# Kernel tuning notes

Hardware: AMD Instinct MI355X
Metric: run time of the kernel (lower is better)

The kernel has to match this reference:

```python
import jax, jax.numpy as jnp
import numpy as np

B, T, C, H, N = 4, 4096, 1024, 16, 64
D_DECAY, D_AAA, D_MV, D_GATE = 64, 64, 32, 160
EPS_GN = 1e-5 * 8 ** 2  # GroupNorm eps = 1e-5 * head_size_divisor**2


def _k(i):
    return jax.random.fold_in(jax.random.key(0), i)


def setup_inputs():
    p = {}
    p["x"] = jax.random.normal(_k(1), (B, T, C), jnp.float32)
    p["v_first"] = jax.random.normal(_k(2), (B, T, C), jnp.float32)
    for i, name in enumerate(["x_r", "x_w", "x_k", "x_v", "x_a", "x_g"]):
        p[name] = jax.random.uniform(_k(10 + i), (1, 1, C), jnp.float32)
    p["w0"] = jnp.linspace(-7.0, -2.0, C, dtype=jnp.float32).reshape(1, 1, C) + 0.5
    p["w1"] = jax.random.normal(_k(20), (C, D_DECAY), jnp.float32) * 0.02
    p["w2"] = jax.random.normal(_k(21), (D_DECAY, C), jnp.float32) * 0.02
    p["a0"] = jax.random.normal(_k(22), (1, 1, C), jnp.float32) * 0.02
    p["a1"] = jax.random.normal(_k(23), (C, D_AAA), jnp.float32) * 0.02
    p["a2"] = jax.random.normal(_k(24), (D_AAA, C), jnp.float32) * 0.02
    p["v0"] = jnp.ones((1, 1, C), jnp.float32)
    p["v1"] = jax.random.normal(_k(25), (C, D_MV), jnp.float32) * 0.02
    p["v2"] = jax.random.normal(_k(26), (D_MV, C), jnp.float32) * 0.02
    p["g1"] = jax.random.normal(_k(27), (C, D_GATE), jnp.float32) * 0.02
    p["g2"] = jax.random.normal(_k(28), (D_GATE, C), jnp.float32) * 0.02
    p["k_k"] = jnp.full((1, 1, C), 0.85, jnp.float32)
    p["k_a"] = jnp.ones((1, 1, C), jnp.float32)
    p["r_k"] = jax.random.normal(_k(29), (H, N), jnp.float32) * 0.02
    s = 0.5 / C ** 0.5
    p["Wr"] = jax.random.uniform(_k(30), (C, C), jnp.float32, -s, s)
    p["Wk"] = jax.random.uniform(_k(31), (C, C), jnp.float32, -0.1 * s, 0.1 * s)
    p["Wv"] = jax.random.uniform(_k(32), (C, C), jnp.float32, -s, s)
    p["Wo"] = jax.random.uniform(_k(33), (C, C), jnp.float32, -s, s)
    p["ln_w"] = jnp.ones((C,), jnp.float32)
    p["ln_b"] = jnp.zeros((C,), jnp.float32)
    p["alpha"] = jnp.array(0.5, jnp.float32)
    return p


def _wkv_scan(ins, reverse):
    # ins: tuple of time-major (T,B,H,N) arrays: r, decay, k, v, a, b
    def step(S, inp):
        r_t, d_t, k_t, v_t, a_t, b_t = inp
        sa = jnp.einsum('bhij,bhj->bhi', S, a_t)  # in-context removal term
        S = (S * d_t[:, :, None, :]
             + sa[..., None] * b_t[:, :, None, :]
             + v_t[..., None] * k_t[:, :, None, :])
        return S, jnp.einsum('bhij,bhj->bhi', S, r_t)
    S0 = jnp.zeros((B, H, N, N), jnp.float32)
    return jax.lax.scan(step, S0, ins, reverse=reverse)[1]


def reference(x, v_first, x_r, x_w, x_k, x_v, x_a, x_g, w0, w1, w2, a0, a1, a2,
              v0, v1, v2, g1, g2, k_k, k_a, r_k, Wr, Wk, Wv, Wo, ln_w, ln_b, alpha):
    xx = jnp.pad(x, ((0, 0), (1, 0), (0, 0)))[:, :T, :] - x  # token shift
    xr = x + xx * x_r
    xw = x + xx * x_w
    xk = x + xx * x_k
    xv = x + xx * x_v
    xa = x + xx * x_a
    xg = x + xx * x_g
    r = xr @ Wr.T
    w = -jax.nn.softplus(-(w0 + jnp.tanh(xw @ w1) @ w2)) - 0.5
    k = xk @ Wk.T
    v = xv @ Wv.T
    v = v + (v_first - v) * jax.nn.sigmoid(v0 + (xv @ v1) @ v2)  # layer_id != 0
    a = jax.nn.sigmoid(a0 + (xa @ a1) @ a2)
    g = jax.nn.sigmoid(xg @ g1) @ g2
    kk = (k * k_k).reshape(B, T, H, N)
    kk = kk / jnp.maximum(jnp.linalg.norm(kk, axis=-1, keepdims=True), 1e-12)
    k = k * (1.0 + (a - 1.0) * k_a)
    rh = r.reshape(B, T, H, N)
    kh = k.reshape(B, T, H, N)
    vh = v.reshape(B, T, H, N)
    dec = jnp.exp(-jnp.exp(w.reshape(B, T, H, N)))  # per-channel decay
    ah = -kk
    bh = kk * a.reshape(B, T, H, N)
    tm = lambda z: jnp.transpose(z, (1, 0, 2, 3))  # -> (T,B,H,N)
    ins = (tm(rh), tm(dec), tm(kh), tm(vh), tm(ah), tm(bh))
    y_f = _wkv_scan(ins, reverse=False)
    y_b = _wkv_scan(ins, reverse=True)
    y = alpha * y_f + (1.0 - alpha) * y_b  # bidirectional blend (alpha)
    y = jnp.transpose(y, (1, 0, 2, 3))  # (B,T,H,N)
    mu = y.mean(-1, keepdims=True)
    var = y.var(-1, keepdims=True)
    y = (y - mu) / jnp.sqrt(var + EPS_GN)  # GroupNorm(H groups)
    y = y * ln_w.reshape(1, 1, H, N) + ln_b.reshape(1, 1, H, N)
    y = y + (rh * kh * r_k).sum(-1, keepdims=True) * vh
    out = (y.reshape(B, T, C) * g) @ Wo.T
    return (out, v_first)
```

## Files before the change

### kernel.cpp

```cpp
#include <hip/hip_runtime.h>
#include <hip/hip_bf16.h>
#include <math.h>

#define BB 4
#define TT 4096
#define CC 1024
#define HH 16
#define NN 64
#define BT (BB*TT)
#define EPS_GN 6.4e-4f
#define TMAX (TT-1)
#define LCH 64
#define CB 8
#define NB 8
#define STR 68

typedef __attribute__((ext_vector_type(8))) short bf16x8;
typedef __attribute__((ext_vector_type(4))) float f32x4;

__device__ __forceinline__ float sigmoidf_(float x) {
    return 1.0f / (1.0f + expf(-x));
}

__device__ __forceinline__ float waveReduceSum(float v) {
    #pragma unroll
    for (int off = 32; off > 0; off >>= 1)
        v += __shfl_xor(v, off, 64);
    return v;
}

__device__ __forceinline__ unsigned short f2bf(float f) {
    unsigned u = __float_as_uint(f);
    u += 0x7FFFu + ((u >> 16) & 1u);
    return (unsigned short)(u >> 16);
}
__device__ __forceinline__ float bf2f(unsigned short h) {
    return __uint_as_float(((unsigned)h) << 16);
}

__device__ __forceinline__ void gll16(const unsigned short* g, unsigned short* l) {
    __builtin_amdgcn_global_load_lds(
        (__attribute__((address_space(1))) void*)(g),
        (__attribute__((address_space(3))) void*)(l), 16, 0, 0);
}

template<int SA0,int SA1,int SB0,int SB1>
__device__ __forceinline__ void gemm64(const float* __restrict__ A,
                                       const float* __restrict__ B,
                                       float acc[4][4], int tr, int tc) {
    #pragma unroll 2
    for (int kx = 0; kx < 64; kx += 4) {
        float a_[4][4];
        if (SA0 == 1) {
            #pragma unroll
            for (int kk = 0; kk < 4; kk++) {
                float4 t = *(const float4*)&A[tr + (kx + kk) * SA1];
                a_[0][kk] = t.x; a_[1][kk] = t.y; a_[2][kk] = t.z; a_[3][kk] = t.w;
            }
        } else {
            #pragma unroll
            for (int r = 0; r < 4; r++) {
                float4 t = *(const float4*)&A[(tr + r) * SA0 + kx];
                a_[r][0] = t.x; a_[r][1] = t.y; a_[r][2] = t.z; a_[r][3] = t.w;
            }
        }
        float b_[4][4];
        if (SB0 == 1) {
            #pragma unroll
            for (int kk = 0; kk < 4; kk++) {
                float4 t = *(const float4*)&B[tc + (kx + kk) * SB1];
                b_[0][kk] = t.x; b_[1][kk] = t.y; b_[2][kk] = t.z; b_[3][kk] = t.w;
            }
        } else {
            #pragma unroll
            for (int cq = 0; cq < 4; cq++) {
                float4 t = *(const float4*)&B[(tc + cq) * SB0 + kx];
                b_[cq][0] = t.x; b_[cq][1] = t.y; b_[cq][2] = t.z; b_[cq][3] = t.w;
            }
        }
        #pragma unroll
        for (int r = 0; r < 4; r++)
            #pragma unroll
            for (int cq = 0; cq < 4; cq++)
                #pragma unroll
                for (int kk = 0; kk < 4; kk++)
                    acc[r][cq] = fmaf(a_[r][kk], b_[cq][kk], acc[r][cq]);
    }
}

__global__ __launch_bounds__(256) void conv_split_x3(
    const float* __restrict__ X,
    const float* __restrict__ mr, const float* __restrict__ mk,
    const float* __restrict__ mv,
    unsigned short* __restrict__ rH, unsigned short* __restrict__ rL,
    unsigned short* __restrict__ kH, unsigned short* __restrict__ kL,
    unsigned short* __restrict__ vH, unsigned short* __restrict__ vL)
{
    int g = blockIdx.x * 256 + threadIdx.x;
    int m = g >> 7;
    int k = (g & 127) * 8;
    const float* px = X + (size_t)m * CC + k;
    float xv8[8], pv[8];
    {
        float4 x0 = *(const float4*)px;
        float4 x1 = *(const float4*)(px + 4);
        xv8[0]=x0.x; xv8[1]=x0.y; xv8[2]=x0.z; xv8[3]=x0.w;
        xv8[4]=x1.x; xv8[5]=x1.y; xv8[6]=x1.z; xv8[7]=x1.w;
    }
    if ((m & (TT - 1)) == 0) {
        #pragma unroll
        for (int j = 0; j < 8; j++) pv[j] = 0.f;
    } else {
        float4 p0 = *(const float4*)(px - CC);
        float4 p1 = *(const float4*)(px - CC + 4);
        pv[0]=p0.x; pv[1]=p0.y; pv[2]=p0.z; pv[3]=p0.w;
        pv[4]=p1.x; pv[5]=p1.y; pv[6]=p1.z; pv[7]=p1.w;
    }
    const float* mixes[3] = {mr, mk, mv};
    unsigned short* His[3] = {rH, kH, vH};
    unsigned short* Los[3] = {rL, kL, vL};
    #pragma unroll
    for (int s = 0; s < 3; s++) {
        float4 m0 = *(const float4*)(mixes[s] + k);
        float4 m1 = *(const float4*)(mixes[s] + k + 4);
        float mv8[8] = {m0.x,m0.y,m0.z,m0.w,m1.x,m1.y,m1.z,m1.w};
        unsigned short hi[8], lo[8];
        #pragma unroll
        for (int j = 0; j < 8; j++) {
            float a = xv8[j] + (pv[j] - xv8[j]) * mv8[j];
            hi[j] = f2bf(a);
            lo[j] = f2bf(a - bf2f(hi[j]));
        }
        uint4 H, L;
        H.x = (unsigned)hi[0] | ((unsigned)hi[1] << 16);
        H.y = (unsigned)hi[2] | ((unsigned)hi[3] << 16);
        H.z = (unsigned)hi[4] | ((unsigned)hi[5] << 16);
        H.w = (unsigned)hi[6] | ((unsigned)hi[7] << 16);
        L.x = (unsigned)lo[0] | ((unsigned)lo[1] << 16);
        L.y = (unsigned)lo[2] | ((unsigned)lo[3] << 16);
        L.z = (unsigned)lo[4] | ((unsigned)lo[5] << 16);
        L.w = (unsigned)lo[6] | ((unsigned)lo[7] << 16);
        *(uint4*)(His[s] + (size_t)g * 8) = H;
        *(uint4*)(Los[s] + (size_t)g * 8) = L;
    }
}


__global__ __launch_bounds__(256) void conv_w4(
    const float* __restrict__ Wr, const float* __restrict__ Wk,
    const float* __restrict__ Wv, const float* __restrict__ Wo,
    unsigned short* __restrict__ Hi, unsigned short* __restrict__ Lo)
{
    int g = blockIdx.x * 256 + threadIdx.x;
    int y = blockIdx.y;
    const float* W = (y == 0) ? Wr : (y == 1) ? Wk : (y == 2) ? Wv : Wo;
    size_t doff = (size_t)y * CC * CC;
    int m = g >> 7;
    int k = (g & 127) * 8;
    const float* px = W + (size_t)m * CC + k;
    float a[8];
    {
        float4 x0 = *(const float4*)px;
        float4 x1 = *(const float4*)(px + 4);
        a[0]=x0.x; a[1]=x0.y; a[2]=x0.z; a[3]=x0.w;
        a[4]=x1.x; a[5]=x1.y; a[6]=x1.z; a[7]=x1.w;
    }
    unsigned short hi[8], lo[8];
    #pragma unroll
    for (int j = 0; j < 8; j++) {
        hi[j] = f2bf(a[j]);
        lo[j] = f2bf(a[j] - bf2f(hi[j]));
    }
    uint4 H, L;
    H.x = (unsigned)hi[0] | ((unsigned)hi[1] << 16);
    H.y = (unsigned)hi[2] | ((unsigned)hi[3] << 16);
    H.z = (unsigned)hi[4] | ((unsigned)hi[5] << 16);
    H.w = (unsigned)hi[6] | ((unsigned)hi[7] << 16);
    L.x = (unsigned)lo[0] | ((unsigned)lo[1] << 16);
    L.y = (unsigned)lo[2] | ((unsigned)lo[3] << 16);
    L.z = (unsigned)lo[4] | ((unsigned)lo[5] << 16);
    L.w = (unsigned)lo[6] | ((unsigned)lo[7] << 16);
    *(uint4*)(Hi + doff + (size_t)g * 8) = H;
    *(uint4*)(Lo + doff + (size_t)g * 8) = L;
}

__global__ __launch_bounds__(256) void conv_w2(
    const float* __restrict__ W, int K, int Kp,
    unsigned short* __restrict__ Hi, unsigned short* __restrict__ Lo)
{
    int idx = blockIdx.x * 256 + threadIdx.x;
    int nk8 = Kp >> 3;
    if (idx >= CC * nk8) return;
    int n = idx / nk8, k0 = (idx - n * nk8) * 8;
    unsigned short h8[8], l8[8];
    #pragma unroll
    for (int j = 0; j < 8; j++) {
        int k = k0 + j;
        float v = (k < K) ? W[(size_t)k * CC + n] : 0.f;
        h8[j] = f2bf(v);
        l8[j] = f2bf(v - bf2f(h8[j]));
    }
    uint4 H, L;
    H.x = (unsigned)h8[0] | ((unsigned)h8[1] << 16);
    H.y = (unsigned)h8[2] | ((unsigned)h8[3] << 16);
    H.z = (unsigned)h8[4] | ((unsigned)h8[5] << 16);
    H.w = (unsigned)h8[6] | ((unsigned)h8[7] << 16);
    L.x = (unsigned)l8[0] | ((unsigned)l8[1] << 16);
    L.y = (unsigned)l8[2] | ((unsigned)l8[3] << 16);
    L.z = (unsigned)l8[4] | ((unsigned)l8[5] << 16);
    L.w = (unsigned)l8[6] | ((unsigned)l8[7] << 16);
    *(uint4*)(Hi + (size_t)n * Kp + k0) = H;
    *(uint4*)(Lo + (size_t)n * Kp + k0) = L;
}

__global__ __launch_bounds__(256, 3) void gemm_split_bf16(
    const unsigned short* __restrict__ A0h, const unsigned short* __restrict__ A0l,
    const unsigned short* __restrict__ A1h, const unsigned short* __restrict__ A1l,
    const unsigned short* __restrict__ A2h, const unsigned short* __restrict__ A2l,
    const unsigned short* __restrict__ W4h, const unsigned short* __restrict__ W4l,
    float* __restrict__ O0, float* __restrict__ O1, float* __restrict__ O2,
    int wbase)
{
    __shared__ __align__(16) unsigned short lds[4][128 * 32];
    const int sel = blockIdx.y;
    const unsigned short* Ah = (sel == 0) ? A0h : (sel == 1) ? A1h : A2h;
    const unsigned short* Al = (sel == 0) ? A0l : (sel == 1) ? A1l : A2l;
    float* Out = (sel == 0) ? O0 : (sel == 1) ? O1 : O2;
    const unsigned short* Bh = W4h + (size_t)(wbase + sel) * CC * CC;
    const unsigned short* Bl = W4l + (size_t)(wbase + sel) * CC * CC;
    const int tid = threadIdx.x, lane = tid & 63, wave = tid >> 6;
    const int wm = (wave >> 1) * 64, wn = (wave & 1) * 64;
    const int wg = blockIdx.x;
    const int xcd = wg & 7;
    const int j = wg >> 3;
    const int m0 = ((j >> 3) * 8 + xcd) * 128;
    const int n0 = (j & 7) * 128;

    f32x4 acc[4][4];
    #pragma unroll
    for (int i = 0; i < 4; i++)
        #pragma unroll
        for (int jj = 0; jj < 4; jj++)
            acc[i][jj] = (f32x4){0.f, 0.f, 0.f, 0.f};

    for (int k0 = 0; k0 < CC; k0 += 32) {
        #pragma unroll
        for (int p = 0; p < 4; p++) {
            const unsigned short* sbase = (p == 0) ? Ah : (p == 1) ? Al
                                        : (p == 2) ? Bh : Bl;
            const int rbase = (p < 2) ? m0 : n0;
            #pragma unroll
            for (int i = 0; i < 2; i++) {
                int slot = i * 256 + wave * 64 + lane;
                int row = slot >> 2, gsl = slot & 3;
                const unsigned short* src = sbase
                    + (size_t)(rbase + row) * CC + k0 + ((gsl ^ (row & 3)) * 8);
                gll16(src, &lds[p][(size_t)(i * 256 + wave * 64) * 8]);
            }
        }
        __syncthreads();

        const int gk = lane >> 4;
        bf16x8 bhf[4], blf[4];
        #pragma unroll
        for (int nt = 0; nt < 4; nt++) {
            int col = wn + nt * 16 + (lane & 15);
            int el = col * 32 + ((gk ^ (col & 3)) * 8);
            bhf[nt] = *(const bf16x8*)&lds[2][el];
            blf[nt] = *(const bf16x8*)&lds[3][el];
        }
        #pragma unroll
        for (int mt = 0; mt < 4; mt++) {
            int row = wm + mt * 16 + (lane & 15);
            int el = row * 32 + ((gk ^ (row & 3)) * 8);
            bf16x8 ahf = *(const bf16x8*)&lds[0][el];
            bf16x8 alf = *(const bf16x8*)&lds[1][el];
            #pragma unroll
            for (int nt = 0; nt < 4; nt++) {
                acc[mt][nt] = __builtin_amdgcn_mfma_f32_16x16x32_bf16(
                    ahf, bhf[nt], acc[mt][nt], 0, 0, 0);
                acc[mt][nt] = __builtin_amdgcn_mfma_f32_16x16x32_bf16(
                    alf, bhf[nt], acc[mt][nt], 0, 0, 0);
                acc[mt][nt] = __builtin_amdgcn_mfma_f32_16x16x32_bf16(
                    ahf, blf[nt], acc[mt][nt], 0, 0, 0);
            }
        }
        __syncthreads();
    }
    #pragma unroll
    for (int mt = 0; mt < 4; mt++)
        #pragma unroll
        for (int nt = 0; nt < 4; nt++) {
            int col = n0 + wn + nt * 16 + (lane & 15);
            #pragma unroll
            for (int r = 0; r < 4; r++) {
                int row = m0 + wm + mt * 16 + (lane >> 4) * 4 + r;
                Out[(size_t)row * CC + col] = acc[mt][nt][r];
            }
        }
}

__global__ __launch_bounds__(256) void lora1_all(
    const float* __restrict__ X,
    const float* __restrict__ w1, const float* __restrict__ a1,
    const float* __restrict__ v1, const float* __restrict__ g1,
    const float* __restrict__ xw, const float* __restrict__ xa,
    const float* __restrict__ xv, const float* __restrict__ xg,
    unsigned short* __restrict__ awh, unsigned short* __restrict__ awl,
    unsigned short* __restrict__ aah, unsigned short* __restrict__ aal,
    unsigned short* __restrict__ avh, unsigned short* __restrict__ avl,
    unsigned short* __restrict__ agh, unsigned short* __restrict__ agl)
{
    const int y = blockIdx.y;
    const float* W; const float* mix; unsigned short *Hi, *Lo;
    int Ncols, n0, epi, Kp;
    if (y == 0)      { W=w1; mix=xw; Hi=awh; Lo=awl; Ncols=64;  n0=0;          epi=1; Kp=64;  }
    else if (y == 1) { W=a1; mix=xa; Hi=aah; Lo=aal; Ncols=64;  n0=0;          epi=0; Kp=64;  }
    else if (y == 2) { W=v1; mix=xv; Hi=avh; Lo=avl; Ncols=32;  n0=0;          epi=0; Kp=64;  }
    else             { W=g1; mix=xg; Hi=agh; Lo=agl; Ncols=160; n0=(y-3)*64;   epi=2; Kp=192; }

    __shared__ float As[8][64];
    __shared__ float Bs[8][64];
    const int tid = threadIdx.x;
    const int m0 = blockIdx.x * 64;
    const int sr  = tid >> 1;
    const int skq = (tid & 1) * 4;
    const int t2  = tid - 128;
    const int bkr = t2 >> 4;
    const int bnq = (t2 & 15) * 4;
    const int tm = (tid >> 3) * 2;
    const int tn = (tid & 7) * 8;

    float acc[2][8];
    #pragma unroll
    for (int i = 0; i < 2; i++)
        #pragma unroll
        for (int j = 0; j < 8; j++) acc[i][j] = 0.f;

    auto ldAm = [&](int gm, int gk) -> float4 {
        const float* px = X + (size_t)gm * CC + gk;
        float4 xvv = *(const float4*)px;
        float4 pv;
        if ((gm & (TT - 1)) == 0) pv = make_float4(0.f, 0.f, 0.f, 0.f);
        else pv = *(const float4*)(px - CC);
        float4 mv = *(const float4*)(mix + gk);
        xvv.x += (pv.x - xvv.x) * mv.x;
        xvv.y += (pv.y - xvv.y) * mv.y;
        xvv.z += (pv.z - xvv.z) * mv.z;
        xvv.w += (pv.w - xvv.w) * mv.w;
        return xvv;
    };

    float4 aR = make_float4(0.f, 0.f, 0.f, 0.f);
    float4 bR = make_float4(0.f, 0.f, 0.f, 0.f);
    if (tid < 128) {
        aR = ldAm(m0 + sr, skq);
    } else {
        int gn = n0 + bnq;
        bR = (gn < Ncols) ? *(const float4*)(W + (size_t)bkr * Ncols + gn)
                          : make_float4(0.f, 0.f, 0.f, 0.f);
    }

    for (int k0 = 0; k0 < CC; k0 += 8) {
        __syncthreads();
        if (tid < 128) {
            As[skq + 0][sr] = aR.x;
            As[skq + 1][sr] = aR.y;
            As[skq + 2][sr] = aR.z;
            As[skq + 3][sr] = aR.w;
        } else {
            *(float4*)&Bs[bkr][bnq] = bR;
        }
        __syncthreads();

        if (k0 + 8 < CC) {
            if (tid < 128) {
                aR = ldAm(m0 + sr, k0 + 8 + skq);
            } else {
                int gn = n0 + bnq;
                bR = (gn < Ncols) ? *(const float4*)(W + (size_t)(k0 + 8 + bkr) * Ncols + gn)
                                  : make_float4(0.f, 0.f, 0.f, 0.f);
            }
        }

        #pragma unroll
        for (int kk = 0; kk < 8; ++kk) {
            float av[2], bv[8];
            av[0] = As[kk][tm];
            av[1] = As[kk][tm + 1];
            *(float4*)&bv[0] = *(const float4*)&Bs[kk][tn];
            *(float4*)&bv[4] = *(const float4*)&Bs[kk][tn + 4];
            #pragma unroll
            for (int i = 0; i < 2; i++)
                #pragma unroll
                for (int j = 0; j < 8; j++)
                    acc[i][j] = fmaf(av[i], bv[j], acc[i][j]);
        }
    }

    #pragma unroll
    for (int i = 0; i < 2; i++) {
        int gm = m0 + tm + i;
        int gn = n0 + tn;
        if (gn < Kp) {
            unsigned short h8[8], l8[8];
            #pragma unroll
            for (int j = 0; j < 8; j++) {
                float v = 0.f;
                if (gn + j < Ncols) {
                    v = acc[i][j];
                    if (epi == 1) v = tanhf(v);
                    else if (epi == 2) v = sigmoidf_(v);
                }
                h8[j] = f2bf(v);
                l8[j] = f2bf(v - bf2f(h8[j]));
            }
            uint4 H, L;
            H.x = (unsigned)h8[0] | ((unsigned)h8[1] << 16);
            H.y = (unsigned)h8[2] | ((unsigned)h8[3] << 16);
            H.z = (unsigned)h8[4] | ((unsigned)h8[5] << 16);
            H.w = (unsigned)h8[6] | ((unsigned)h8[7] << 16);
            L.x = (unsigned)l8[0] | ((unsigned)l8[1] << 16);
            L.y = (unsigned)l8[2] | ((unsigned)l8[3] << 16);
            L.z = (unsigned)l8[4] | ((unsigned)l8[5] << 16);
            L.w = (unsigned)l8[6] | ((unsigned)l8[7] << 16);
            *(uint4*)(Hi + (size_t)gm * Kp + gn) = H;
            *(uint4*)(Lo + (size_t)gm * Kp + gn) = L;
        }
    }
}

__global__ __launch_bounds__(256, 3) void lora2_mfma(
    const unsigned short* __restrict__ awh, const unsigned short* __restrict__ awl,
    const unsigned short* __restrict__ aah, const unsigned short* __restrict__ aal,
    const unsigned short* __restrict__ avh, const unsigned short* __restrict__ avl,
    const unsigned short* __restrict__ agh, const unsigned short* __restrict__ agl,
    const unsigned short* __restrict__ w2h, const unsigned short* __restrict__ w2l,
    const unsigned short* __restrict__ a2h, const unsigned short* __restrict__ a2l,
    const unsigned short* __restrict__ v2h, const unsigned short* __restrict__ v2l,
    const unsigned short* __restrict__ g2h, const unsigned short* __restrict__ g2l,
    const float* __restrict__ w0, const float* __restrict__ a0v,
    const float* __restrict__ v0v, const float* __restrict__ v_first,
    float* __restrict__ decb, float* __restrict__ ab,
    float* __restrict__ vbuf, float* __restrict__ gb)
{
    __shared__ __align__(16) unsigned short lds[24576];
    const int z = blockIdx.z;
    const unsigned short *Ah, *Al, *Bh, *Bl; int Kp;
    if (z == 0)      { Ah = awh; Al = awl; Bh = w2h; Bl = w2l; Kp = 64;  }
    else if (z == 1) { Ah = aah; Al = aal; Bh = a2h; Bl = a2l; Kp = 64;  }
    else if (z == 2) { Ah = avh; Al = avl; Bh = v2h; Bl = v2l; Kp = 64;  }
    else             { Ah = agh; Al = agl; Bh = g2h; Bl = g2l; Kp = 192; }

    const int tid = threadIdx.x, lane = tid & 63, wave = tid >> 6;
    const int wm = (wave >> 1) * 64, wn = (wave & 1) * 32;
    const int m0 = blockIdx.x * 128, n0 = blockIdx.y * 64;

    f32x4 acc[4][2];
    #pragma unroll
    for (int i = 0; i < 4; i++)
        #pragma unroll
        for (int jj = 0; jj < 2; jj++)
            acc[i][jj] = (f32x4){0.f, 0.f, 0.f, 0.f};

    for (int k0 = 0; k0 < Kp; k0 += 64) {
        #pragma unroll
        for (int p = 0; p < 2; p++) {
            const unsigned short* sbase = (p == 0) ? Ah : Al;
            #pragma unroll
            for (int i = 0; i < 4; i++) {
                int slot = i * 256 + wave * 64 + lane;
                int row = slot >> 3, gsl = slot & 7;
                const unsigned short* src = sbase
                    + (size_t)(m0 + row) * Kp + k0 + ((gsl ^ (row & 7)) * 8);
                gll16(src, &lds[(size_t)(p * 8192) + (size_t)(i * 256 + wave * 64) * 8]);
            }
        }
        #pragma unroll
        for (int p = 0; p < 2; p++) {
            const unsigned short* sbase = (p == 0) ? Bh : Bl;
            #pragma unroll
            for (int i = 0; i < 2; i++) {
                int slot = i * 256 + wave * 64 + lane;
                int row = slot >> 3, gsl = slot & 7;
                const unsigned short* src = sbase
                    + (size_t)(n0 + row) * Kp + k0 + ((gsl ^ (row & 7)) * 8);
                gll16(src, &lds[(size_t)(16384 + p * 4096) + (size_t)(i * 256 + wave * 64) * 8]);
            }
        }
        __syncthreads();

        #pragma unroll
        for (int ks = 0; ks < 2; ks++) {
            bf16x8 bhf[2], blf[2];
            #pragma unroll
            for (int nt = 0; nt < 2; nt++) {
                int col = wn + nt * 16 + (lane & 15);
                int gk = ks * 4 + (lane >> 4);
                int el = col * 64 + ((gk ^ (col & 7)) * 8);
                bhf[nt] = *(const bf16x8*)&lds[16384 + el];
                blf[nt] = *(const bf16x8*)&lds[20480 + el];
            }
            #pragma unroll
            for (int mt = 0; mt < 4; mt++) {
                int row = wm + mt * 16 + (lane & 15);
                int gk = ks * 4 + (lane >> 4);
                int el = row * 64 + ((gk ^ (row & 7)) * 8);
                bf16x8 ahf = *(const bf16x8*)&lds[el];
                bf16x8 alf = *(const bf16x8*)&lds[8192 + el];
                #pragma unroll
                for (int nt = 0; nt < 2; nt++) {
                    acc[mt][nt] = __builtin_amdgcn_mfma_f32_16x16x32_bf16(
                        ahf, bhf[nt], acc[mt][nt], 0, 0, 0);
                    acc[mt][nt] = __builtin_amdgcn_mfma_f32_16x16x32_bf16(
                        alf, bhf[nt], acc[mt][nt], 0, 0, 0);
                    acc[mt][nt] = __builtin_amdgcn_mfma_f32_16x16x32_bf16(
                        ahf, blf[nt], acc[mt][nt], 0, 0, 0);
                }
            }
        }
        __syncthreads();
    }
    float* cf = (float*)&lds[0];
    #pragma unroll
    for (int mt = 0; mt < 4; mt++)
        #pragma unroll
        for (int nt = 0; nt < 2; nt++)
            #pragma unroll
            for (int r = 0; r < 4; r++) {
                int row = wm + mt * 16 + (lane >> 4) * 4 + r;
                int col = wn + nt * 16 + (lane & 15);
                cf[row * 68 + col] = acc[mt][nt][r];
            }
    __syncthreads();
    #pragma unroll
    for (int i = 0; i < 8; i++) {
        int idx = tid + 256 * i;
        int row = idx >> 4, c4 = (idx & 15) * 4;
        float4 v = *(float4*)&cf[row * 68 + c4];
        int gm = m0 + row;
        int c = n0 + c4;
        size_t off = (size_t)gm * CC + c;
        if (z == 0) {
            float4 w0q = *(const float4*)(w0 + c);
            float4 o;
            o.x = expf(-expf(-log1pf(expf(-(w0q.x + v.x))) - 0.5f));
            o.y = expf(-expf(-log1pf(expf(-(w0q.y + v.y))) - 0.5f));
            o.z = expf(-expf(-log1pf(expf(-(w0q.z + v.z))) - 0.5f));
            o.w = expf(-expf(-log1pf(expf(-(w0q.w + v.w))) - 0.5f));
            *(float4*)&decb[off] = o;
        } else if (z == 1) {
            float4 a0q = *(const float4*)(a0v + c);
            float4 o;
            o.x = sigmoidf_(a0q.x + v.x);
            o.y = sigmoidf_(a0q.y + v.y);
            o.z = sigmoidf_(a0q.z + v.z);
            o.w = sigmoidf_(a0q.w + v.w);
            *(float4*)&ab[off] = o;
        } else if (z == 2) {
            float4 v0q = *(const float4*)(v0v + c);
            float4 vr = *(const float4*)&vbuf[off];
            float4 vf = *(const float4*)&v_first[off];
            float4 o;
            o.x = vr.x + (vf.x - vr.x) * sigmoidf_(v0q.x + v.x);
            o.y = vr.y + (vf.y - vr.y) * sigmoidf_(v0q.y + v.y);
            o.z = vr.z + (vf.z - vr.z) * sigmoidf_(v0q.z + v.z);
            o.w = vr.w + (vf.w - vr.w) * sigmoidf_(v0q.w + v.w);
            *(float4*)&vbuf[off] = o;
        } else {
            *(float4*)&gb[off] = v;
        }
    }
}

__global__ __launch_bounds__(256) void wkvA(
    const float* __restrict__ kb, const float* __restrict__ ab,
    const float* __restrict__ vb, const float* __restrict__ decb,
    const float* __restrict__ k_k, const float* __restrict__ k_a,
    float* __restrict__ Gb, float* __restrict__ Ub,
    float* __restrict__ Bpb, float* __restrict__ Kpb,
    float* __restrict__ wcb, int cb)
{
    __shared__ __align__(16) float sAp[64 * STR];
    __shared__ __align__(16) float sBp[64 * STR];
    __shared__ __align__(16) float sKp[64 * STR];
    __shared__ __align__(16) float sT [64 * STR];
    __shared__ float sSeg[4][64];
    const int inst = blockIdx.x;
    const int bhd = inst >> 3, lc = inst & 7;
    const int dir = bhd & 1, bh = bhd >> 1, b = bh >> 4, h = bh & 15;
    const int c64 = (cb * CB + lc) * LCH;
    const int tid = threadIdx.x;
    const int lane = tid & 63, seg = tid >> 6;
    const int ch = h * 64 + lane;
    const size_t gbase = (size_t)inst * 4096;

    float loc[16];
    {
        float run = 1.f;
        #pragma unroll
        for (int i = 0; i < 16; i++) {
            int p = seg * 16 + i;
            int t = dir ? (TMAX - (c64 + p)) : (c64 + p);
            float d = decb[((size_t)(b * TT + t)) * CC + ch];
            run *= d; loc[i] = run;
        }
        sSeg[seg][lane] = run;
    }
    __syncthreads();
    float pre = 1.f;
    for (int s2 = 0; s2 < seg; ++s2) pre *= sSeg[s2][lane];
    {
        const float kkl = k_k[ch], kal = k_a[ch];
        #pragma unroll
        for (int i = 0; i < 16; i++) {
            int p = seg * 16 + i;
            int t = dir ? (TMAX - (c64 + p)) : (c64 + p);
            size_t ra = ((size_t)(b * TT + t)) * CC + ch;
            float kraw = kb[ra], asig = ab[ra];
            float kkv = kraw * kkl;
            float s2 = waveReduceSum(kkv * kkv);
            float kkn = kkv / fmaxf(sqrtf(s2), 1e-12f);
            float wc = loc[i] * pre;
            float wx = (i == 0) ? pre : loc[i - 1] * pre;
            float apv = -kkn * wx;
            float bpv = kkn * asig / wc;
            float kpv = kraw * (1.f + (asig - 1.f) * kal) / wc;
            sAp[lane * STR + p] = apv;
            sBp[lane * STR + p] = bpv;
            sKp[lane * STR + p] = kpv;
            Bpb[gbase + p * 64 + lane] = bpv;
            Kpb[gbase + p * 64 + lane] = kpv;
            wcb[gbase + p * 64 + lane] = wc;
        }
    }
    __syncthreads();

    const int tr = (tid >> 4) * 4, tc = (tid & 15) * 4;
    {
        float acc[4][4] = {};
        gemm64<1, STR, 1, STR>(sAp, sKp, acc, tr, tc);
        #pragma unroll
        for (int r = 0; r < 4; r++)
            #pragma unroll
            for (int cq = 0; cq < 4; cq++)
                sT[(tr + r) * STR + tc + cq] = (tc + cq < tr + r) ? acc[r][cq] : 0.f;
    }
    __syncthreads();
    {
        float accY[4][4] = {};
        const float* vbase = vb + ((size_t)(b * TT + (dir ? (TMAX - c64) : c64))) * CC
                           + h * 64 + tc;
        const ptrdiff_t vstep = dir ? -(ptrdiff_t)CC : (ptrdiff_t)CC;
        #pragma unroll 2
        for (int j4 = 0; j4 < 64; j4 += 4) {
            float a_[4][4];
            #pragma unroll
            for (int r = 0; r < 4; r++) {
                float4 t4 = *(const float4*)&sT[(tr + r) * STR + j4];
                a_[r][0] = t4.x; a_[r][1] = t4.y; a_[r][2] = t4.z; a_[r][3] = t4.w;
            }
            float4 vq[4];
            #pragma unroll
            for (int kk = 0; kk < 4; kk++)
                vq[kk] = *(const float4*)(vbase + (ptrdiff_t)(j4 + kk) * vstep);
            #pragma unroll
            for (int r = 0; r < 4; r++) {
                accY[r][0] = fmaf(a_[r][0], vq[0].x, fmaf(a_[r][1], vq[1].x,
                             fmaf(a_[r][2], vq[2].x, fmaf(a_[r][3], vq[3].x, accY[r][0]))));
                accY[r][1] = fmaf(a_[r][0], vq[0].y, fmaf(a_[r][1], vq[1].y,
                             fmaf(a_[r][2], vq[2].y, fmaf(a_[r][3], vq[3].y, accY[r][1]))));
                accY[r][2] = fmaf(a_[r][0], vq[0].z, fmaf(a_[r][1], vq[1].z,
                             fmaf(a_[r][2], vq[2].z, fmaf(a_[r][3], vq[3].z, accY[r][2]))));
                accY[r][3] = fmaf(a_[r][0], vq[0].w, fmaf(a_[r][1], vq[1].w,
                             fmaf(a_[r][2], vq[2].w, fmaf(a_[r][3], vq[3].w, accY[r][3]))));
            }
        }
        #pragma unroll
        for (int r = 0; r < 4; r++)
            #pragma unroll
            for (int cq = 0; cq < 4; cq++)
                sKp[(tr + r) * STR + tc + cq] = accY[r][cq];
    }
    __syncthreads();
    {
        float acc[4][4] = {};
        gemm64<1, STR, 1, STR>(sAp, sBp, acc, tr, tc);
        #pragma unroll
        for (int r = 0; r < 4; r++)
            #pragma unroll
            for (int cq = 0; cq < 4; cq++)
                sT[(tr + r) * STR + tc + cq] = (tc + cq < tr + r) ? acc[r][cq] : 0.f;
    }
    __syncthreads();
    if (tid < 64) {
        for (int r = 0; r < 64; ++r) {
            float acc = 0.f;
            for (int s = 0; s < r; ++s)
                acc = fmaf(sT[r * STR + s], sBp[s * STR + tid], acc);
            sBp[r * STR + tid] = (r == tid) ? 1.f : acc;
        }
    }
    __syncthreads();
    {
        float accG[4][4] = {};
        gemm64<STR, 1, STR, 1>(sBp, sAp, accG, tr, tc);
        float accU[4][4] = {};
        gemm64<STR, 1, 1, STR>(sBp, sKp, accU, tr, tc);
        #pragma unroll
        for (int r = 0; r < 4; r++) {
            *(float4*)&Gb[gbase + (tr + r) * 64 + tc] =
                make_float4(accG[r][0], accG[r][1], accG[r][2], accG[r][3]);
            *(float4*)&Ub[gbase + (tr + r) * 64 + tc] =
                make_float4(accU[r][0], accU[r][1], accU[r][2], accU[r][3]);
        }
    }
}

__global__ __launch_bounds__(256) void wkvB(
    const float* __restrict__ vb,
    const float* __restrict__ Gb, float* __restrict__ Ub,
    const float* __restrict__ Bpb, const float* __restrict__ Kpb,
    const float* __restrict__ wcb, float* __restrict__ S0b,
    float* __restrict__ Scur, int cb)
{
    __shared__ __align__(16) float sS[64 * STR];
    __shared__ __align__(16) float sG[64 * STR];
    __shared__ __align__(16) float sU[64 * STR];
    __shared__ __align__(16) float sB[64 * STR];
    __shared__ __align__(16) float sK[64 * STR];
    __shared__ __align__(16) float sV[64 * STR];
    const int bhd = blockIdx.x;
    const int dir = bhd & 1, bh = bhd >> 1, b = bh >> 4, h = bh & 15;
    const int tid = threadIdx.x;
    const int tr = (tid >> 4) * 4, tc = (tid & 15) * 4;

    for (int i = tid; i < 4096; i += 256)
        sS[(i >> 6) * STR + (i & 63)] = Scur[(size_t)bhd * 4096 + i];
    __syncthreads();

    for (int lc = 0; lc < CB; ++lc) {
        const int inst = bhd * CB + lc;
        const size_t gbase = (size_t)inst * 4096;
        const int c64 = (cb * CB + lc) * LCH;
        for (int i = tid; i < 4096; i += 256) {
            int rr = i >> 6, jj = i & 63;
            sG[rr * STR + jj] = Gb[gbase + i];
            sB[rr * STR + jj] = Bpb[gbase + i];
            sK[rr * STR + jj] = Kpb[gbase + i];
            int t = dir ? (TMAX - (c64 + rr)) : (c64 + rr);
            sV[rr * STR + jj] = vb[((size_t)(b * TT + t)) * CC + h * 64 + jj];
            S0b[gbase + i] = sS[rr * STR + jj];
        }
        __syncthreads();
        {
            float acc[4][4];
            #pragma unroll
            for (int r = 0; r < 4; r++) {
                float4 u0 = *(const float4*)&Ub[gbase + (tr + r) * 64 + tc];
                acc[r][0] = u0.x; acc[r][1] = u0.y; acc[r][2] = u0.z; acc[r][3] = u0.w;
            }
            gemm64<STR, 1, STR, 1>(sG, sS, acc, tr, tc);
            #pragma unroll
            for (int r = 0; r < 4; r++) {
                #pragma unroll
                for (int cq = 0; cq < 4; cq++) sU[(tr + r) * STR + tc + cq] = acc[r][cq];
                *(float4*)&Ub[gbase + (tr + r) * 64 + tc] =
                    make_float4(acc[r][0], acc[r][1], acc[r][2], acc[r][3]);
            }
        }
        __syncthreads();
        {
            float acc[4][4] = {};
            gemm64<1, STR, 1, STR>(sU, sB, acc, tr, tc);
            gemm64<1, STR, 1, STR>(sV, sK, acc, tr, tc);
            float w63[4];
            #pragma unroll
            for (int cq = 0; cq < 4; cq++) w63[cq] = wcb[gbase + 63 * 64 + tc + cq];
            #pragma unroll
            for (int r = 0; r < 4; r++)
                #pragma unroll
                for (int cq = 0; cq < 4; cq++) {
                    float sv = sS[(tr + r) * STR + tc + cq];
                    acc[r][cq] = (sv + acc[r][cq]) * w63[cq];
                }
            #pragma unroll
            for (int r = 0; r < 4; r++)
                #pragma unroll
                for (int cq = 0; cq < 4; cq++)
                    sS[(tr + r) * STR + tc + cq] = acc[r][cq];
        }
        __syncthreads();
    }
    for (int i = tid; i < 4096; i += 256)
        Scur[(size_t)bhd * 4096 + i] = sS[(i >> 6) * STR + (i & 63)];
}

__global__ __launch_bounds__(256) void wkvC(
    const float* __restrict__ rb, const float* __restrict__ vb,
    const float* __restrict__ Bpb, const float* __restrict__ Kpb,
    const float* __restrict__ Ub, const float* __restrict__ S0b,
    const float* __restrict__ wcb, const float* __restrict__ alpha_p,
    float* __restrict__ yb, int cb)
{
    __shared__ __align__(16) float sR[64 * STR];
    __shared__ __align__(16) float sO[64 * STR];
    __shared__ __align__(16) float sT2[64 * STR];
    const int inst = blockIdx.x;
    const int bhd = inst >> 3, lc = inst & 7;
    const int dir = bhd & 1, bh = bhd >> 1, b = bh >> 4, h = bh & 15;
    const int c64 = (cb * CB + lc) * LCH;
    const int tid = threadIdx.x, lane = tid & 63, seg = tid >> 6;
    const size_t gbase = (size_t)inst * 4096;
    const float alpha = alpha_p[0];
    const float wscale = dir ? (1.f - alpha) : alpha;
    const bool first = (cb < NB / 2);

    #pragma unroll
    for (int i = 0; i < 16; i++) {
        int p = seg * 16 + i;
        int t = dir ? (TMAX - (c64 + p)) : (c64 + p);
        size_t ra = ((size_t)(b * TT + t)) * CC + h * 64 + lane;
        float wc = wcb[gbase + p * 64 + lane];
        sR[lane * STR + p] = rb[ra] * wc;
        sO[lane * STR + p] = Bpb[gbase + p * 64 + lane];
    }
    __syncthreads();
    const int tr = (tid >> 4) * 4, tc = (tid & 15) * 4;
    float accO[4][4] = {};
    {
        float acc[4][4] = {};
        gemm64<1, STR, 1, STR>(sR, sO, acc, tr, tc);
        #pragma unroll
        for (int r = 0; r < 4; r++)
            #pragma unroll
            for (int cq = 0; cq < 4; cq++)
                sT2[(tr + r) * STR + tc + cq] = (tc + cq <= tr + r) ? acc[r][cq] : 0.f;
    }
    __syncthreads();
    for (int i = tid; i < 4096; i += 256)
        sO[(i >> 6) * STR + (i & 63)] = Ub[gbase + i];
    __syncthreads();
    gemm64<STR, 1, 1, STR>(sT2, sO, accO, tr, tc);
    __syncthreads();
    #pragma unroll
    for (int i = 0; i < 16; i++) {
        int p = seg * 16 + i;
        sO[lane * STR + p] = Kpb[gbase + p * 64 + lane];
    }
    __syncthreads();
    {
        float acc[4][4] = {};
        gemm64<1, STR, 1, STR>(sR, sO, acc, tr, tc);
        #pragma unroll
        for (int r = 0; r < 4; r++)
            #pragma unroll
            for (int cq = 0; cq < 4; cq++)
                sT2[(tr + r) * STR + tc + cq] = (tc + cq <= tr + r) ? acc[r][cq] : 0.f;
    }
    __syncthreads();
    #pragma unroll
    for (int i = 0; i < 16; i++) {
        int p = seg * 16 + i;
        int t = dir ? (TMAX - (c64 + p)) : (c64 + p);
        sO[p * STR + lane] = vb[((size_t)(b * TT + t)) * CC + h * 64 + lane];
    }
    __syncthreads();
    gemm64<STR, 1, 1, STR>(sT2, sO, accO, tr, tc);
    __syncthreads();
    for (int i = tid; i < 4096; i += 256)
        sO[(i >> 6) * STR + (i & 63)] = S0b[gbase + i];
    __syncthreads();
    gemm64<1, STR, STR, 1>(sR, sO, accO, tr, tc);
    #pragma unroll
    for (int r = 0; r < 4; r++) {
        int p = tr + r;
        int t = dir ? (TMAX - (c64 + p)) : (c64 + p);
        float* yp = &yb[((size_t)(b * TT + t)) * CC + h * 64 + tc];
        float4 o;
        if (first) {
            o.x = wscale * accO[r][0];
            o.y = wscale * accO[r][1];
            o.z = wscale * accO[r][2];
            o.w = wscale * accO[r][3];
        } else {
            float4 old = *(float4*)yp;
            o.x = old.x + wscale * accO[r][0];
            o.y = old.y + wscale * accO[r][1];
            o.z = old.z + wscale * accO[r][2];
            o.w = old.w + wscale * accO[r][3];
        }
        *(float4*)yp = o;
    }
}

__global__ __launch_bounds__(256) void post_kernel(
    const float* __restrict__ yb, const float* __restrict__ rbv,
    const float* __restrict__ kbv, const float* __restrict__ abv,
    const float* __restrict__ vbv, const float* __restrict__ gbv,
    const float* __restrict__ kaw, const float* __restrict__ r_k,
    const float* __restrict__ ln_w, const float* __restrict__ ln_b,
    unsigned short* __restrict__ zh, unsigned short* __restrict__ zl)
{
    const int t = blockIdx.x;
    const int tid = threadIdx.x;
    const size_t base = (size_t)t * CC;
    #pragma unroll
    for (int j = 0; j < 4; j++) {
        int c = tid + 256 * j;
        float y = yb[base + c];
        float s1 = waveReduceSum(y);
        float s2 = waveReduceSum(y * y);
        float mu = s1 * (1.0f / 64.0f);
        float var = s2 * (1.0f / 64.0f) - mu * mu;
        float yn = (y - mu) * rsqrtf(var + EPS_GN);
        yn = yn * ln_w[c] + ln_b[c];
        float rv = rbv[base + c];
        float kf = kbv[base + c] * (1.0f + (abv[base + c] - 1.0f) * kaw[c]);
        float vv = vbv[base + c];
        float dot = waveReduceSum(rv * kf * r_k[c]);
        yn += dot * vv;
        float z = yn * gbv[base + c];
        unsigned short h = f2bf(z);
        zh[base + c] = h;
        zl[base + c] = f2bf(z - bf2f(h));
    }
}

extern "C" void kernel_launch(void* const* d_in, const int* in_sizes, int n_in,
                              void* d_out, int out_size, void* d_ws, size_t ws_size,
                              hipStream_t stream)
{
    (void)in_sizes; (void)n_in; (void)out_size; (void)ws_size;
    const float* x      = (const float*)d_in[0];
    const float* vfirst = (const float*)d_in[1];
    const float* x_r    = (const float*)d_in[2];
    const float* x_w    = (const float*)d_in[3];
    const float* x_k    = (const float*)d_in[4];
    const float* x_v    = (const float*)d_in[5];
    const float* x_a    = (const float*)d_in[6];
    const float* x_g    = (const float*)d_in[7];
    const float* w0     = (const float*)d_in[8];
    const float* w1     = (const float*)d_in[9];
    const float* w2     = (const float*)d_in[10];
    const float* a0     = (const float*)d_in[11];
    const float* a1     = (const float*)d_in[12];
    const float* a2     = (const float*)d_in[13];
    const float* v0     = (const float*)d_in[14];
    const float* v1     = (const float*)d_in[15];
    const float* v2     = (const float*)d_in[16];
    const float* g1     = (const float*)d_in[17];
    const float* g2     = (const float*)d_in[18];
    const float* k_k    = (const float*)d_in[19];
    const float* k_a    = (const float*)d_in[20];
    const float* r_k    = (const float*)d_in[21];
    const float* Wr     = (const float*)d_in[22];
    const float* Wk     = (const float*)d_in[23];
    const float* Wv     = (const float*)d_in[24];
    const float* Wo     = (const float*)d_in[25];
    const float* ln_w   = (const float*)d_in[26];
    const float* ln_b   = (const float*)d_in[27];
    const float* alpha  = (const float*)d_in[28];

    const size_t SZ = (size_t)BT * CC;
    const size_t CHB = (size_t)1024 * 4096;
    float* ws   = (float*)d_ws;
    float* rb   = ws + 0 * SZ;
    float* kb   = ws + 1 * SZ;
    float* vb   = ws + 2 * SZ;
    float* decb = ws + 3 * SZ;
    float* ab   = ws + 4 * SZ;
    float* actf = ws + 5 * SZ;
    unsigned short* awh = (unsigned short*)actf;
    unsigned short* awl = awh + (size_t)BT * 64;
    unsigned short* aah = awl + (size_t)BT * 64;
    unsigned short* aal = aah + (size_t)BT * 64;
    unsigned short* avh = aal + (size_t)BT * 64;
    unsigned short* avl = avh + (size_t)BT * 64;
    unsigned short* agh = avl + (size_t)BT * 64;
    unsigned short* agl = agh + (size_t)BT * 192;
    float* Gb   = actf + (size_t)BT * 384;
    float* Ub   = Gb + CHB;
    float* Bpb  = Ub + CHB;
    float* Kpb  = Bpb + CHB;
    float* S0b  = Kpb + CHB;
    float* wcb  = S0b + CHB;
    float* Scur = wcb + CHB;
    unsigned short* W4h = (unsigned short*)(Scur + (size_t)128 * 4096);
    unsigned short* W4l = W4h + (size_t)CC * CC * 4;
    unsigned short* w2th = W4l + (size_t)CC * CC * 4;
    unsigned short* w2tl = w2th + (size_t)CC * 64;
    unsigned short* a2th = w2tl + (size_t)CC * 64;
    unsigned short* a2tl = a2th + (size_t)CC * 64;
    unsigned short* v2th = a2tl + (size_t)CC * 64;
    unsigned short* v2tl = v2th + (size_t)CC * 64;
    unsigned short* g2th = v2tl + (size_t)CC * 64;
    unsigned short* g2tl = g2th + (size_t)CC * 192;
    float* outp = (float*)d_out;
    unsigned short* xrh = (unsigned short*)outp;
    unsigned short* xrl = xrh + SZ;
    unsigned short* xkh = xrl + SZ;
    unsigned short* xkl = xkh + SZ;
    unsigned short* xvh = (unsigned short*)decb;
    unsigned short* xvl = xvh + SZ;
    float* gb   = outp;
    float* yb   = outp + SZ;
    unsigned short* zAh = (unsigned short*)decb;
    unsigned short* zAl = zAh + SZ;

    dim3 blk(256);
    const int NG_A = BT * (CC / 8);
    dim3 gridA(NG_A / 256);

    conv_split_x3<<<gridA, blk, 0, stream>>>(x, x_r, x_k, x_v,
                                             xrh, xrl, xkh, xkl, xvh, xvl);
    conv_w4<<<dim3(512, 4), blk, 0, stream>>>(Wr, Wk, Wv, Wo, W4h, W4l);
    gemm_split_bf16<<<dim3(1024, 3), blk, 0, stream>>>(
        xrh, xrl, xkh, xkl, xvh, xvl, W4h, W4l, rb, kb, vb, 0);

    conv_w2<<<dim3(32), blk, 0, stream>>>(w2, 64, 64, w2th, w2tl);
    conv_w2<<<dim3(32), blk, 0, stream>>>(a2, 64, 64, a2th, a2tl);
    conv_w2<<<dim3(32), blk, 0, stream>>>(v2, 32, 64, v2th, v2tl);
    conv_w2<<<dim3(96), blk, 0, stream>>>(g2, 160, 192, g2th, g2tl);

    lora1_all<<<dim3(BT / 64, 6), blk, 0, stream>>>(x, w1, a1, v1, g1,
        x_w, x_a, x_v, x_g, awh, awl, aah, aal, avh, avl, agh, agl);
    lora2_mfma<<<dim3(BT / 128, CC / 64, 4), blk, 0, stream>>>(
        awh, awl, aah, aal, avh, avl, agh, agl,
        w2th, w2tl, a2th, a2tl, v2th, v2tl, g2th, g2tl,
        w0, a0, v0, vfirst, decb, ab, vb, gb);

    hipMemsetAsync(Scur, 0, (size_t)128 * 4096 * sizeof(float), stream);
    for (int cb = 0; cb < NB; ++cb) {
        wkvA<<<dim3(1024), blk, 0, stream>>>(kb, ab, vb, decb, k_k, k_a,
                                             Gb, Ub, Bpb, Kpb, wcb, cb);
        wkvB<<<dim3(128), blk, 0, stream>>>(vb, Gb, Ub, Bpb, Kpb, wcb, S0b, Scur, cb);
        wkvC<<<dim3(1024), blk, 0, stream>>>(rb, vb, Bpb, Kpb, Ub, S0b, wcb,
                                             alpha, yb, cb);
    }

    post_kernel<<<dim3(BT), blk, 0, stream>>>(yb, rb, kb, ab, vb, gb, k_a, r_k,
                                              ln_w, ln_b, zAh, zAl);
    hipMemcpyAsync(outp + SZ, vfirst, SZ * sizeof(float),
                   hipMemcpyDeviceToDevice, stream);
    gemm_split_bf16<<<dim3(1024, 1), blk, 0, stream>>>(
        zAh, zAl, zAh, zAl, zAh, zAl, W4h, W4l, outp, outp, outp, 3);
}
```

Baseline: 3.139 ms.

## Replace serial triangular solve with doubling series and widen state-pass blocks

In wkvA, the forward substitution that inverts the unit-lower-triangular matrix ran on only 64 threads. It is replaced by a product-of-powers expansion (I+T)(I+T^2)(I+T^4)... computed with block-wide 64x64 GEMMs over five doubling iterations, so all 256 threads take part. In wkvB the block grows from 256 to 512 threads, each computing a 2x4 tile through a new gemm64h helper, with an added barrier before the state write-back. This gives the sequential chunk-state pass more parallelism per block, at the cost of more FLOPs and barriers in wkvA, and the series reorders floating-point summation.

```diff
diff --git a/kernel.cpp b/kernel.cpp
--- a/kernel.cpp
+++ b/kernel.cpp
@@ -80,6 +80,50 @@
         }
         #pragma unroll
         for (int r = 0; r < 4; r++)
+            #pragma unroll
+            for (int cq = 0; cq < 4; cq++)
+                #pragma unroll
+                for (int kk = 0; kk < 4; kk++)
+                    acc[r][cq] = fmaf(a_[r][kk], b_[cq][kk], acc[r][cq]);
+    }
+}
+
+template<int SA0,int SA1,int SB0,int SB1>
+__device__ __forceinline__ void gemm64h(const float* __restrict__ A,
+                                        const float* __restrict__ B,
+                                        float acc[2][4], int tr, int tc) {
+    #pragma unroll 2
+    for (int kx = 0; kx < 64; kx += 4) {
+        float a_[2][4];
+        if (SA0 == 1) {
+            #pragma unroll
+            for (int kk = 0; kk < 4; kk++) {
+                float2 t = *(const float2*)&A[tr + (kx + kk) * SA1];
+                a_[0][kk] = t.x; a_[1][kk] = t.y;
+            }
+        } else {
+            #pragma unroll
+            for (int r = 0; r < 2; r++) {
+                float4 t = *(const float4*)&A[(tr + r) * SA0 + kx];
+                a_[r][0] = t.x; a_[r][1] = t.y; a_[r][2] = t.z; a_[r][3] = t.w;
+            }
+        }
+        float b_[4][4];
+        if (SB0 == 1) {
+            #pragma unroll
+            for (int kk = 0; kk < 4; kk++) {
+                float4 t = *(const float4*)&B[tc + (kx + kk) * SB1];
+                b_[0][kk] = t.x; b_[1][kk] = t.y; b_[2][kk] = t.z; b_[3][kk] = t.w;
+            }
+        } else {
+            #pragma unroll
+            for (int cq = 0; cq < 4; cq++) {
+                float4 t = *(const float4*)&B[(tc + cq) * SB0 + kx];
+                b_[cq][0] = t.x; b_[cq][1] = t.y; b_[cq][2] = t.z; b_[cq][3] = t.w;
+            }
+        }
+        #pragma unroll
+        for (int r = 0; r < 2; r++)
             #pragma unroll
             for (int cq = 0; cq < 4; cq++)
                 #pragma unroll
@@ -144,7 +188,6 @@
         *(uint4*)(Los[s] + (size_t)g * 8) = L;
     }
 }
-
 
 __global__ __launch_bounds__(256) void conv_w4(
     const float* __restrict__ Wr, const float* __restrict__ Wk,
@@ -693,15 +736,36 @@
                 sT[(tr + r) * STR + tc + cq] = (tc + cq < tr + r) ? acc[r][cq] : 0.f;
     }
     __syncthreads();
-    if (tid < 64) {
-        for (int r = 0; r < 64; ++r) {
-            float acc = 0.f;
-            for (int s = 0; s < r; ++s)
-                acc = fmaf(sT[r * STR + s], sBp[s * STR + tid], acc);
-            sBp[r * STR + tid] = (r == tid) ? 1.f : acc;
-        }
-    }
-    __syncthreads();
+    {
+        #pragma unroll
+        for (int r = 0; r < 4; r++)
+            #pragma unroll
+            for (int cq = 0; cq < 4; cq++) {
+                int gi = tr + r, gj = tc + cq;
+                sBp[gi * STR + gj] = ((gi == gj) ? 1.f : 0.f) + sT[gi * STR + gj];
+            }
+    }
+    __syncthreads();
+    for (int it = 0; it < 5; ++it) {
+        float accY[4][4] = {};
+        gemm64<STR, 1, 1, STR>(sT, sT, accY, tr, tc);
+        __syncthreads();
+        #pragma unroll
+        for (int r = 0; r < 4; r++)
+            #pragma unroll
+            for (int cq = 0; cq < 4; cq++)
+                sT[(tr + r) * STR + tc + cq] = accY[r][cq];
+        __syncthreads();
+        float accR[4][4] = {};
+        gemm64<STR, 1, 1, STR>(sBp, sT, accR, tr, tc);
+        __syncthreads();
+        #pragma unroll
+        for (int r = 0; r < 4; r++)
+            #pragma unroll
+            for (int cq = 0; cq < 4; cq++)
+                sBp[(tr + r) * STR + tc + cq] += accR[r][cq];
+        __syncthreads();
+    }
     {
         float accG[4][4] = {};
         gemm64<STR, 1, STR, 1>(sBp, sAp, accG, tr, tc);
@@ -717,7 +781,7 @@
     }
 }
 
-__global__ __launch_bounds__(256) void wkvB(
+__global__ __launch_bounds__(512) void wkvB(
     const float* __restrict__ vb,
     const float* __restrict__ Gb, float* __restrict__ Ub,
     const float* __restrict__ Bpb, const float* __restrict__ Kpb,
@@ -733,9 +797,9 @@
     const int bhd = blockIdx.x;
     const int dir = bhd & 1, bh = bhd >> 1, b = bh >> 4, h = bh & 15;
     const int tid = threadIdx.x;
-    const int tr = (tid >> 4) * 4, tc = (tid & 15) * 4;
-
-    for (int i = tid; i < 4096; i += 256)
+    const int tr = (tid >> 4) * 2, tc = (tid & 15) * 4;
+
+    for (int i = tid; i < 4096; i += 512)
         sS[(i >> 6) * STR + (i & 63)] = Scur[(size_t)bhd * 4096 + i];
     __syncthreads();
 
@@ -743,7 +807,7 @@
         const int inst = bhd * CB + lc;
         const size_t gbase = (size_t)inst * 4096;
         const int c64 = (cb * CB + lc) * LCH;
-        for (int i = tid; i < 4096; i += 256) {
+        for (int i = tid; i < 4096; i += 512) {
             int rr = i >> 6, jj = i & 63;
             sG[rr * STR + jj] = Gb[gbase + i];
             sB[rr * STR + jj] = Bpb[gbase + i];
@@ -754,15 +818,15 @@
         }
         __syncthreads();
         {
-            float acc[4][4];
-            #pragma unroll
-            for (int r = 0; r < 4; r++) {
+            float acc[2][4];
+            #pragma unroll
+            for (int r = 0; r < 2; r++) {
                 float4 u0 = *(const float4*)&Ub[gbase + (tr + r) * 64 + tc];
                 acc[r][0] = u0.x; acc[r][1] = u0.y; acc[r][2] = u0.z; acc[r][3] = u0.w;
             }
-            gemm64<STR, 1, STR, 1>(sG, sS, acc, tr, tc);
-            #pragma unroll
-            for (int r = 0; r < 4; r++) {
+            gemm64h<STR, 1, STR, 1>(sG, sS, acc, tr, tc);
+            #pragma unroll
+            for (int r = 0; r < 2; r++) {
                 #pragma unroll
                 for (int cq = 0; cq < 4; cq++) sU[(tr + r) * STR + tc + cq] = acc[r][cq];
                 *(float4*)&Ub[gbase + (tr + r) * 64 + tc] =
@@ -771,28 +835,29 @@
         }
         __syncthreads();
         {
-            float acc[4][4] = {};
-            gemm64<1, STR, 1, STR>(sU, sB, acc, tr, tc);
-            gemm64<1, STR, 1, STR>(sV, sK, acc, tr, tc);
+            float acc[2][4] = {};
+            gemm64h<1, STR, 1, STR>(sU, sB, acc, tr, tc);
+            gemm64h<1, STR, 1, STR>(sV, sK, acc, tr, tc);
             float w63[4];
             #pragma unroll
             for (int cq = 0; cq < 4; cq++) w63[cq] = wcb[gbase + 63 * 64 + tc + cq];
             #pragma unroll
-            for (int r = 0; r < 4; r++)
+            for (int r = 0; r < 2; r++)
                 #pragma unroll
                 for (int cq = 0; cq < 4; cq++) {
                     float sv = sS[(tr + r) * STR + tc + cq];
                     acc[r][cq] = (sv + acc[r][cq]) * w63[cq];
                 }
-            #pragma unroll
-            for (int r = 0; r < 4; r++)
+            __syncthreads();
+            #pragma unroll
+            for (int r = 0; r < 2; r++)
                 #pragma unroll
                 for (int cq = 0; cq < 4; cq++)
                     sS[(tr + r) * STR + tc + cq] = acc[r][cq];
         }
         __syncthreads();
     }
-    for (int i = tid; i < 4096; i += 256)
+    for (int i = tid; i < 4096; i += 512)
         Scur[(size_t)bhd * 4096 + i] = sS[(i >> 6) * STR + (i & 63)];
 }
 
@@ -1034,7 +1099,7 @@
     for (int cb = 0; cb < NB; ++cb) {
         wkvA<<<dim3(1024), blk, 0, stream>>>(kb, ab, vb, decb, k_k, k_a,
                                              Gb, Ub, Bpb, Kpb, wcb, cb);
-        wkvB<<<dim3(128), blk, 0, stream>>>(vb, Gb, Ub, Bpb, Kpb, wcb, S0b, Scur, cb);
+        wkvB<<<dim3(128), dim3(512), 0, stream>>>(vb, Gb, Ub, Bpb, Kpb, wcb, S0b, Scur, cb);
         wkvC<<<dim3(1024), blk, 0, stream>>>(rb, vb, Bpb, Kpb, Ub, S0b, wcb,
                                              alpha, yb, cb);
     }
```

Result: slower. 3.239 ms (+3.2%).

## Cut wkvA shared memory to three tiles to fit three blocks per CU

Applied to the files above, without the earlier changes.

wkvA now uses three 64x68 LDS tiles instead of four and declares launch bounds of three blocks per CU. To make room, the computation is reordered: the A·B product is built first, K is kept in registers and copied into the reused tile afterwards, and the A tile is written to global memory (Gb) and read back from there for the final G gemm. This aims to raise occupancy and overlap latency in the chunked WKV prep kernel. The cost is extra global writes and reads, more barriers, and a risk of register spills under the tighter launch bound.

```diff
diff --git a/kernel.cpp b/kernel.cpp
--- a/kernel.cpp
+++ b/kernel.cpp
@@ -144,7 +144,6 @@
         *(uint4*)(Los[s] + (size_t)g * 8) = L;
     }
 }
-
 
 __global__ __launch_bounds__(256) void conv_w4(
     const float* __restrict__ Wr, const float* __restrict__ Wk,
@@ -573,7 +572,7 @@
     }
 }
 
-__global__ __launch_bounds__(256) void wkvA(
+__global__ __launch_bounds__(256, 3) void wkvA(
     const float* __restrict__ kb, const float* __restrict__ ab,
     const float* __restrict__ vb, const float* __restrict__ decb,
     const float* __restrict__ k_k, const float* __restrict__ k_a,
@@ -581,10 +580,9 @@
     float* __restrict__ Bpb, float* __restrict__ Kpb,
     float* __restrict__ wcb, int cb)
 {
-    __shared__ __align__(16) float sAp[64 * STR];
-    __shared__ __align__(16) float sBp[64 * STR];
-    __shared__ __align__(16) float sKp[64 * STR];
-    __shared__ __align__(16) float sT [64 * STR];
+    __shared__ __align__(16) float sA[64 * STR];
+    __shared__ __align__(16) float sO[64 * STR];
+    __shared__ __align__(16) float sT[64 * STR];
     __shared__ float sSeg[4][64];
     const int inst = blockIdx.x;
     const int bhd = inst >> 3, lc = inst & 7;
@@ -610,6 +608,7 @@
     __syncthreads();
     float pre = 1.f;
     for (int s2 = 0; s2 < seg; ++s2) pre *= sSeg[s2][lane];
+    float kreg[16];
     {
         const float kkl = k_k[ch], kal = k_a[ch];
         #pragma unroll
@@ -626,9 +625,10 @@
             float apv = -kkn * wx;
             float bpv = kkn * asig / wc;
             float kpv = kraw * (1.f + (asig - 1.f) * kal) / wc;
-            sAp[lane * STR + p] = apv;
-            sBp[lane * STR + p] = bpv;
-            sKp[lane * STR + p] = kpv;
+            sA[lane * STR + p] = apv;
+            sO[lane * STR + p] = bpv;
+            kreg[i] = kpv;
+            Gb[gbase + p * 64 + lane] = apv;
             Bpb[gbase + p * 64 + lane] = bpv;
             Kpb[gbase + p * 64 + lane] = kpv;
             wcb[gbase + p * 64 + lane] = wc;
@@ -639,12 +639,27 @@
     const int tr = (tid >> 4) * 4, tc = (tid & 15) * 4;
     {
         float acc[4][4] = {};
-        gemm64<1, STR, 1, STR>(sAp, sKp, acc, tr, tc);
+        gemm64<1, STR, 1, STR>(sA, sO, acc, tr, tc);
         #pragma unroll
         for (int r = 0; r < 4; r++)
             #pragma unroll
             for (int cq = 0; cq < 4; cq++)
                 sT[(tr + r) * STR + tc + cq] = (tc + cq < tr + r) ? acc[r][cq] : 0.f;
+    }
+    __syncthreads();
+    #pragma unroll
+    for (int i = 0; i < 16; i++)
+        sO[lane * STR + seg * 16 + i] = kreg[i];
+    __syncthreads();
+    {
+        float acc[4][4] = {};
+        gemm64<1, STR, 1, STR>(sA, sO, acc, tr, tc);
+        __syncthreads();
+        #pragma unroll
+        for (int r = 0; r < 4; r++)
+            #pragma unroll
+            for (int cq = 0; cq < 4; cq++)
+                sA[(tr + r) * STR + tc + cq] = (tc + cq < tr + r) ? acc[r][cq] : 0.f;
     }
     __syncthreads();
     {
@@ -657,7 +672,7 @@
             float a_[4][4];
             #pragma unroll
             for (int r = 0; r < 4; r++) {
-                float4 t4 = *(const float4*)&sT[(tr + r) * STR + j4];
+                float4 t4 = *(const float4*)&sA[(tr + r) * STR + j4];
                 a_[r][0] = t4.x; a_[r][1] = t4.y; a_[r][2] = t4.z; a_[r][3] = t4.w;
             }
             float4 vq[4];
@@ -676,37 +691,29 @@
                              fmaf(a_[r][2], vq[2].w, fmaf(a_[r][3], vq[3].w, accY[r][3]))));
             }
         }
+        __syncthreads();
         #pragma unroll
         for (int r = 0; r < 4; r++)
             #pragma unroll
             for (int cq = 0; cq < 4; cq++)
-                sKp[(tr + r) * STR + tc + cq] = accY[r][cq];
-    }
-    __syncthreads();
-    {
-        float acc[4][4] = {};
-        gemm64<1, STR, 1, STR>(sAp, sBp, acc, tr, tc);
-        #pragma unroll
-        for (int r = 0; r < 4; r++)
-            #pragma unroll
-            for (int cq = 0; cq < 4; cq++)
-                sT[(tr + r) * STR + tc + cq] = (tc + cq < tr + r) ? acc[r][cq] : 0.f;
+                sO[(tr + r) * STR + tc + cq] = accY[r][cq];
     }
     __syncthreads();
     if (tid < 64) {
         for (int r = 0; r < 64; ++r) {
             float acc = 0.f;
             for (int s = 0; s < r; ++s)
-                acc = fmaf(sT[r * STR + s], sBp[s * STR + tid], acc);
-            sBp[r * STR + tid] = (r == tid) ? 1.f : acc;
+                acc = fmaf(sT[r * STR + s], sA[s * STR + tid], acc);
+            sA[r * STR + tid] = (r == tid) ? 1.f : acc;
         }
     }
     __syncthreads();
     {
+        float accU[4][4] = {};
+        gemm64<STR, 1, 1, STR>(sA, sO, accU, tr, tc);
         float accG[4][4] = {};
-        gemm64<STR, 1, STR, 1>(sBp, sAp, accG, tr, tc);
-        float accU[4][4] = {};
-        gemm64<STR, 1, 1, STR>(sBp, sKp, accU, tr, tc);
+        gemm64<STR, 1, 1, 64>(sA, Gb + gbase, accG, tr, tc);
+        __syncthreads();
         #pragma unroll
         for (int r = 0; r < 4; r++) {
             *(float4*)&Gb[gbase + (tr + r) * 64 + tc] =
```

Measured after the change: 3.113 ms. About the same (-0.8%).
